# Kernel optimization log

Measured on AMD Instinct MI355X. Metric: run time of the kernel, lower is better.

## Reference

```python
import jax, jax.numpy as jnp
import numpy as np

B, T, U = 4, 256, 128
EH, PH, JH, V = 1024, 640, 640, 1024


def setup_inputs() -> dict:
    key = jax.random.key(0)
    ks = jax.random.split(key, 8)
    s_e = 1.0 / np.sqrt(EH)
    s_p = 1.0 / np.sqrt(PH)
    s_j = 1.0 / np.sqrt(JH)
    return {
        "enc": jax.random.normal(ks[0], (B, EH, T), jnp.float32),
        "dec": jax.random.normal(ks[1], (B, PH, U), jnp.float32),
        "W_enc": jax.random.uniform(ks[2], (JH, EH), jnp.float32, -s_e, s_e),
        "b_enc": jax.random.uniform(ks[3], (JH,), jnp.float32, -s_e, s_e),
        "W_pred": jax.random.uniform(ks[4], (JH, PH), jnp.float32, -s_p, s_p),
        "b_pred": jax.random.uniform(ks[5], (JH,), jnp.float32, -s_p, s_p),
        "W_out": jax.random.uniform(ks[6], (V, JH), jnp.float32, -s_j, s_j),
        "b_out": jax.random.uniform(ks[7], (V,), jnp.float32, -s_j, s_j),
    }


def reference(enc, dec, W_enc, b_enc, W_pred, b_pred, W_out, b_out):
    # enc: [B, EH, T], dec: [B, PH, U]  (channels-first, as in torch forward)
    # enc projection -> [B, T, JH] (transpose fused into einsum)
    e = jnp.einsum('bht,jh->btj', enc, W_enc) + b_enc
    # pred projection -> [B, U, JH]
    p = jnp.einsum('bhu,jh->buj', dec, W_pred) + b_pred
    # broadcast add -> [B, T, U, JH], ReLU, output projection -> [B, T, U, V]
    h = jax.nn.relu(e[:, :, None, :] + p[:, None, :, :])
    logits = jnp.einsum('btuj,vj->btuv', h, W_out) + b_out
    return jax.nn.log_softmax(logits, axis=-1)
```

## Files before the change

kernel.cpp:

```cpp
#include <hip/hip_runtime.h>
#include <hip/hip_bf16.h>
#include <stdint.h>

#define B_ 4
#define T_ 256
#define U_ 128
#define EH_ 1024
#define PH_ 640
#define JH_ 640
#define V_ 1024
#define KT_ 20

typedef short bf16x8 __attribute__((ext_vector_type(8)));
typedef float f32x4 __attribute__((ext_vector_type(4)));
typedef unsigned short u16;

typedef const __attribute__((address_space(1))) uint32_t cgu32_t;
typedef __attribute__((address_space(3))) uint32_t lu32_t;

__device__ __forceinline__ u16 f2bf(float f) {
  union { float f; uint32_t u; } v;
  v.f = f;
  uint32_t u = v.u;
  return (u16)((u + 0x7FFFu + ((u >> 16) & 1u)) >> 16);
}

__device__ __forceinline__ void gload16(const void* g, void* l) {
  __builtin_amdgcn_global_load_lds((cgu32_t*)g, (lu32_t*)l, 16, 0, 0);
}

#define VMW(n) asm volatile("s_waitcnt vmcnt(" #n ")" ::: "memory")
#define LGKM0  asm volatile("s_waitcnt lgkmcnt(0)" ::: "memory")
#define SCHEDB __builtin_amdgcn_sched_barrier(0)

__global__ void k_transpose_cvt(const float* __restrict__ in, u16* __restrict__ out,
                                int H, int W) {
  __shared__ float tile[32][33];
  int b = blockIdx.z;
  int h0 = blockIdx.y * 32, w0 = blockIdx.x * 32;
  const float* pin = in + (size_t)b * H * W;
  u16* pout = out + (size_t)b * H * W;
  int lw = threadIdx.x & 31, lh = threadIdx.x >> 5;
#pragma unroll
  for (int i = 0; i < 4; i++) {
    int h = lh + i * 8;
    tile[h][lw] = pin[(size_t)(h0 + h) * W + (w0 + lw)];
  }
  __syncthreads();
#pragma unroll
  for (int i = 0; i < 4; i++) {
    int w = lh + i * 8;
    pout[(size_t)(w0 + w) * H + (h0 + lw)] = f2bf(tile[lw][w]);
  }
}

__global__ void k_prep_w(const float* __restrict__ We, const float* __restrict__ Wp,
                         const float* __restrict__ Wo,
                         u16* __restrict__ WeB, u16* __restrict__ WpB,
                         u16* __restrict__ Wpk) {
  int s = blockIdx.x * 256 + threadIdx.x;
  if (s < 163840) {
    int idx = s * 4;
    float4 v = *(const float4*)(We + idx);
    ushort4 o;
    o.x = f2bf(v.x); o.y = f2bf(v.y); o.z = f2bf(v.z); o.w = f2bf(v.w);
    *(ushort4*)(WeB + idx) = o;
  } else if (s < 266240) {
    int idx = (s - 163840) * 4;
    float4 v = *(const float4*)(Wp + idx);
    ushort4 o;
    o.x = f2bf(v.x); o.y = f2bf(v.y); o.z = f2bf(v.z); o.w = f2bf(v.w);
    *(ushort4*)(WpB + idx) = o;
  } else {
    int q = s - 266240;
    int c = q & 1023;
    int g = (q >> 10) & 3;
    int t = q >> 12;
    const float* src = Wo + (size_t)c * JH_ + t * 32 + g * 8;
    float4 a = *(const float4*)src;
    float4 b2 = *(const float4*)(src + 4);
    ushort4 lo, hi;
    lo.x = f2bf(a.x);  lo.y = f2bf(a.y);  lo.z = f2bf(a.z);  lo.w = f2bf(a.w);
    hi.x = f2bf(b2.x); hi.y = f2bf(b2.y); hi.z = f2bf(b2.z); hi.w = f2bf(b2.w);
    u16* d = Wpk + (size_t)q * 8;
    *(ushort4*)d = lo;
    *(ushort4*)(d + 4) = hi;
  }
}

__global__ void k_proj_gemm(const u16* __restrict__ A, const u16* __restrict__ Bm,
                            const float* __restrict__ bias, float* __restrict__ C,
                            int K, int N, size_t strideA, size_t strideC) {
  __shared__ __align__(16) u16 sA[64 * 64];
  __shared__ __align__(16) u16 sB[64 * 64];
  int bb = blockIdx.z;
  const u16* Ab = A + (size_t)bb * strideA;
  float* Cb = C + (size_t)bb * strideC;
  int m0 = blockIdx.x * 64, n0 = blockIdx.y * 64;
  int tid = threadIdx.x;
  int lane = tid & 63, wid = tid >> 6;

  f32x4 acc[2][2] = {};
  for (int kk = 0; kk < K; kk += 64) {
#pragma unroll
    for (int i = 0; i < 2; i++) {
      int c = tid + i * 256;
      int r = c >> 3, kc = c & 7;
      int s = (r << 3) | (kc ^ (r & 7));
      *(bf16x8*)(sA + s * 8) = *(const bf16x8*)(Ab + (size_t)(m0 + r) * K + kk + kc * 8);
      *(bf16x8*)(sB + s * 8) = *(const bf16x8*)(Bm + (size_t)(n0 + r) * K + kk + kc * 8);
    }
    __syncthreads();
    int wr = (wid >> 1) * 32, wc = (wid & 1) * 32;
    int lr = lane & 15, lk = lane >> 4;
#pragma unroll
    for (int ki = 0; ki < 2; ki++) {
      bf16x8 af[2], bq[2];
#pragma unroll
      for (int mf = 0; mf < 2; mf++) {
        int r = wr + mf * 16 + lr;
        int kc = ki * 4 + lk;
        int s = (r << 3) | (kc ^ (r & 7));
        af[mf] = *(const bf16x8*)(sA + s * 8);
      }
#pragma unroll
      for (int nf = 0; nf < 2; nf++) {
        int r = wc + nf * 16 + lr;
        int kc = ki * 4 + lk;
        int s = (r << 3) | (kc ^ (r & 7));
        bq[nf] = *(const bf16x8*)(sB + s * 8);
      }
#pragma unroll
      for (int mf = 0; mf < 2; mf++)
#pragma unroll
        for (int nf = 0; nf < 2; nf++)
          acc[mf][nf] = __builtin_amdgcn_mfma_f32_16x16x32_bf16(af[mf], bq[nf], acc[mf][nf], 0, 0, 0);
    }
    __syncthreads();
  }
  int wr = (wid >> 1) * 32, wc = (wid & 1) * 32;
  int lr = lane & 15, lq = lane >> 4;
#pragma unroll
  for (int nf = 0; nf < 2; nf++) {
    int n = n0 + wc + nf * 16 + lr;
    float bv = bias[n];
#pragma unroll
    for (int mf = 0; mf < 2; mf++) {
#pragma unroll
      for (int r = 0; r < 4; r++) {
        int m = m0 + wr + mf * 16 + lq * 4 + r;
        Cb[(size_t)m * N + n] = acc[mf][nf][r] + bv;
      }
    }
  }
}

__global__ __launch_bounds__(512)
void k_fused(const float* __restrict__ e, const float* __restrict__ p,
             const u16* __restrict__ Wpk, const float* __restrict__ bout,
             float* __restrict__ out) {
  __shared__ __align__(16) u16 sB[2][32768];
  __shared__ __align__(16) u16 sA[4][2048];
  __shared__ __align__(16) float sE[JH_];
  __shared__ float redm[512];
  __shared__ float reds[512];

  int bid = blockIdx.x;
  int btile = bid >> 1, half = bid & 1, b = btile >> 8;
  int tid = threadIdx.x, lane = tid & 63, wn = tid >> 6;
  int lr = lane & 15, lk = lane >> 4;

  const float* eRow = e + (size_t)btile * JH_;
  const float* pRow = p + ((size_t)b * U_ + half * 64) * JH_;
  float* outB = out + ((size_t)btile * U_ + half * 64) * V_;

  int r_ = tid >> 3, kq_ = tid & 7;
  const float* pSrc = pRow + (size_t)r_ * JH_ + kq_ * 4;
  int aw = (kq_ >> 1) * 512 + r_ * 8 + (kq_ & 1) * 4;

  f32x4 acc[4][8] = {};

  auto stage = [&](int t, int c) {
    const u16* s0 = Wpk + (size_t)t * 32768 + (2 * wn) * 512 + lane * 8;
    u16* d0 = &sB[c][(2 * wn) * 512];
#pragma unroll
    for (int g = 0; g < 4; g++) {
      gload16(s0 + g * 8192, d0 + g * 8192);
      gload16(s0 + g * 8192 + 512, d0 + g * 8192 + 512);
    }
  };
  auto build = [&](int t, float4 pv) {
    float4 ev = *(const float4*)(&sE[t * 32 + kq_ * 4]);
    ushort4 hv;
    hv.x = f2bf(fmaxf(pv.x + ev.x, 0.f));
    hv.y = f2bf(fmaxf(pv.y + ev.y, 0.f));
    hv.z = f2bf(fmaxf(pv.z + ev.z, 0.f));
    hv.w = f2bf(fmaxf(pv.w + ev.w, 0.f));
    *(ushort4*)(&sA[t & 3][aw]) = hv;
  };

  for (int i = tid; i < JH_; i += 512) sE[i] = eRow[i];
  stage(0, 0);
  float4 pbuild = *(const float4*)(pSrc);
  float4 pnext  = *(const float4*)(pSrc + 32);
  LGKM0;
  __builtin_amdgcn_s_barrier();
  build(0, pbuild);
  pbuild = pnext;
  asm volatile("s_waitcnt vmcnt(0) lgkmcnt(0)" ::: "memory");
  __builtin_amdgcn_s_barrier();

  for (int t = 0; t < KT_; t++) {
    if (t + 1 < KT_) stage(t + 1, (t + 1) & 1);
    float4 pfut;
    if (t + 2 < KT_) pfut = *(const float4*)(pSrc + (t + 2) * 32);
    if (t + 1 < KT_) { build(t + 1, pbuild); pbuild = pfut; }
    SCHEDB;
    if (t < KT_ - 2) { VMW(9); } else if (t == KT_ - 2) { VMW(8); } else { VMW(0); }
    SCHEDB;
    __builtin_amdgcn_s_barrier();
    const u16* Ab = &sA[t & 3][lk * 512];
    const u16* Bb = &sB[t & 1][lk * 8192 + wn * 1024];
    bf16x8 af[4], bq[8];
#pragma unroll
    for (int mf = 0; mf < 4; mf++)
      af[mf] = *(const bf16x8*)(Ab + (mf * 16 + lr) * 8);
#pragma unroll
    for (int nf = 0; nf < 8; nf++)
      bq[nf] = *(const bf16x8*)(Bb + (nf * 16 + lr) * 8);
    LGKM0; SCHEDB;
    __builtin_amdgcn_s_setprio(1);
#pragma unroll
    for (int mf = 0; mf < 4; mf++)
#pragma unroll
      for (int nf = 0; nf < 8; nf++)
        acc[mf][nf] = __builtin_amdgcn_mfma_f32_16x16x32_bf16(af[mf], bq[nf], acc[mf][nf], 0, 0, 0);
    __builtin_amdgcn_s_setprio(0);
  }

  float bv[8];
#pragma unroll
  for (int nf = 0; nf < 8; nf++) bv[nf] = bout[wn * 128 + nf * 16 + lr];
#pragma unroll
  for (int mf = 0; mf < 4; mf++)
#pragma unroll
    for (int nf = 0; nf < 8; nf++)
#pragma unroll
      for (int r = 0; r < 4; r++)
        acc[mf][nf][r] += bv[nf];

  float gm[4][4];
#pragma unroll
  for (int mf = 0; mf < 4; mf++)
#pragma unroll
    for (int r = 0; r < 4; r++) {
      float m = acc[mf][0][r];
#pragma unroll
      for (int nf = 1; nf < 8; nf++) m = fmaxf(m, acc[mf][nf][r]);
#pragma unroll
      for (int o = 1; o < 16; o <<= 1) m = fmaxf(m, __shfl_xor(m, o, 64));
      gm[mf][r] = m;
    }
  if ((lane & 15) == 0) {
#pragma unroll
    for (int mf = 0; mf < 4; mf++)
#pragma unroll
      for (int r = 0; r < 4; r++)
        redm[(mf * 16 + lk * 4 + r) * 8 + wn] = gm[mf][r];
  }
  __syncthreads();
#pragma unroll
  for (int mf = 0; mf < 4; mf++)
#pragma unroll
    for (int r = 0; r < 4; r++) {
      int row = mf * 16 + lk * 4 + r;
      float m = redm[row * 8];
#pragma unroll
      for (int w = 1; w < 8; w++) m = fmaxf(m, redm[row * 8 + w]);
      gm[mf][r] = m;
    }
  float ls[4][4];
#pragma unroll
  for (int mf = 0; mf < 4; mf++)
#pragma unroll
    for (int r = 0; r < 4; r++) {
      float s = 0.f;
#pragma unroll
      for (int nf = 0; nf < 8; nf++) s += __expf(acc[mf][nf][r] - gm[mf][r]);
#pragma unroll
      for (int o = 1; o < 16; o <<= 1) s += __shfl_xor(s, o, 64);
      ls[mf][r] = s;
    }
  if ((lane & 15) == 0) {
#pragma unroll
    for (int mf = 0; mf < 4; mf++)
#pragma unroll
      for (int r = 0; r < 4; r++)
        reds[(mf * 16 + lk * 4 + r) * 8 + wn] = ls[mf][r];
  }
  __syncthreads();
#pragma unroll
  for (int mf = 0; mf < 4; mf++)
#pragma unroll
    for (int r = 0; r < 4; r++) {
      int row = mf * 16 + lk * 4 + r;
      float s = reds[row * 8];
#pragma unroll
      for (int w = 1; w < 8; w++) s += reds[row * 8 + w];
      ls[mf][r] = gm[mf][r] + __logf(s);
    }
#pragma unroll
  for (int mf = 0; mf < 4; mf++)
#pragma unroll
    for (int nf = 0; nf < 8; nf++)
#pragma unroll
      for (int r = 0; r < 4; r++)
        outB[(size_t)(mf * 16 + lk * 4 + r) * V_ + wn * 128 + nf * 16 + lr] =
            acc[mf][nf][r] - ls[mf][r];
}

extern "C" void kernel_launch(void* const* d_in, const int* in_sizes, int n_in,
                              void* d_out, int out_size, void* d_ws, size_t ws_size,
                              hipStream_t stream) {
  const float* enc    = (const float*)d_in[0];
  const float* dec    = (const float*)d_in[1];
  const float* W_enc  = (const float*)d_in[2];
  const float* b_enc  = (const float*)d_in[3];
  const float* W_pred = (const float*)d_in[4];
  const float* b_pred = (const float*)d_in[5];
  const float* W_out  = (const float*)d_in[6];
  const float* b_out  = (const float*)d_in[7];
  float* out = (float*)d_out;

  char* ws = (char*)d_ws;
  size_t off = 0;
  auto alloc = [&](size_t bytes) {
    void* pp = ws + off;
    off = (off + bytes + 255) & ~(size_t)255;
    return pp;
  };
  u16* encT   = (u16*)alloc((size_t)B_ * T_ * EH_ * 2);
  u16* decT   = (u16*)alloc((size_t)B_ * U_ * PH_ * 2);
  u16* WencB  = (u16*)alloc((size_t)JH_ * EH_ * 2);
  u16* WpredB = (u16*)alloc((size_t)JH_ * PH_ * 2);
  u16* Wpk    = (u16*)alloc((size_t)KT_ * 32768 * 2);
  float* eBuf = (float*)alloc((size_t)B_ * T_ * JH_ * 4);
  float* pBuf = (float*)alloc((size_t)B_ * U_ * JH_ * 4);

  k_transpose_cvt<<<dim3(T_ / 32, EH_ / 32, B_), 256, 0, stream>>>(enc, encT, EH_, T_);
  k_transpose_cvt<<<dim3(U_ / 32, PH_ / 32, B_), 256, 0, stream>>>(dec, decT, PH_, U_);
  k_prep_w<<<1360, 256, 0, stream>>>(W_enc, W_pred, W_out, WencB, WpredB, Wpk);
  k_proj_gemm<<<dim3(T_ / 64, JH_ / 64, B_), 256, 0, stream>>>(
      encT, WencB, b_enc, eBuf, EH_, JH_, (size_t)T_ * EH_, (size_t)T_ * JH_);
  k_proj_gemm<<<dim3(U_ / 64, JH_ / 64, B_), 256, 0, stream>>>(
      decT, WpredB, b_pred, pBuf, PH_, JH_, (size_t)U_ * PH_, (size_t)U_ * JH_);

  k_fused<<<B_ * T_ * 2, 512, 0, stream>>>(eBuf, pBuf, Wpk, b_out, out);
}
```

Before: 329.6 us.

## Load fused-kernel operands directly into registers, dropping LDS staging

The fused joint kernel no longer stages the W_out tiles and the ReLU activations through shared memory. Each wave now loads its W fragments and a repacked p tensor straight from global memory into registers, with double-buffered prefetch. A new pack kernel lays p out so the loads line up with the MFMA fragments, and the bf16 conversion now uses the packed v_cvt_pk_bf16_f32 instruction. This removes the LDS round trips and most barriers, but every wave fetches its own W data from global memory and cache, and register pressure goes up under launch_bounds(512,2).

```diff
diff --git a/kernel.cpp b/kernel.cpp
--- a/kernel.cpp
+++ b/kernel.cpp
@@ -15,9 +15,6 @@
 typedef float f32x4 __attribute__((ext_vector_type(4)));
 typedef unsigned short u16;
 
-typedef const __attribute__((address_space(1))) uint32_t cgu32_t;
-typedef __attribute__((address_space(3))) uint32_t lu32_t;
-
 __device__ __forceinline__ u16 f2bf(float f) {
   union { float f; uint32_t u; } v;
   v.f = f;
@@ -25,13 +22,11 @@
   return (u16)((u + 0x7FFFu + ((u >> 16) & 1u)) >> 16);
 }
 
-__device__ __forceinline__ void gload16(const void* g, void* l) {
-  __builtin_amdgcn_global_load_lds((cgu32_t*)g, (lu32_t*)l, 16, 0, 0);
-}
-
-#define VMW(n) asm volatile("s_waitcnt vmcnt(" #n ")" ::: "memory")
-#define LGKM0  asm volatile("s_waitcnt lgkmcnt(0)" ::: "memory")
-#define SCHEDB __builtin_amdgcn_sched_barrier(0)
+__device__ __forceinline__ uint32_t cvt2(float lo, float hi) {
+  uint32_t r;
+  asm("v_cvt_pk_bf16_f32 %0, %1, %2" : "=v"(r) : "v"(lo), "v"(hi));
+  return r;
+}
 
 __global__ void k_transpose_cvt(const float* __restrict__ in, u16* __restrict__ out,
                                 int H, int W) {
@@ -155,13 +150,23 @@
   }
 }
 
-__global__ __launch_bounds__(512)
-void k_fused(const float* __restrict__ e, const float* __restrict__ p,
-             const u16* __restrict__ Wpk, const float* __restrict__ bout,
-             float* __restrict__ out) {
-  __shared__ __align__(16) u16 sB[2][32768];
-  __shared__ __align__(16) u16 sA[4][2048];
-  __shared__ __align__(16) float sE[JH_];
+__global__ void k_pack_p(const float* __restrict__ pBuf, float* __restrict__ pPk) {
+  int s = blockIdx.x * 256 + threadIdx.x;
+  int m = s & 127;
+  int g = (s >> 7) % 80;
+  int b = (s >> 7) / 80;
+  const float* src = pBuf + ((size_t)b * 128 + m) * JH_ + g * 8;
+  float4 a = *(const float4*)src;
+  float4 c = *(const float4*)(src + 4);
+  float* d = pPk + (size_t)s * 8;
+  *(float4*)d = a;
+  *(float4*)(d + 4) = c;
+}
+
+__global__ __launch_bounds__(512, 2)
+void k_fused_reg(const float* __restrict__ e, const float* __restrict__ pPk,
+                 const u16* __restrict__ Wpk, const float* __restrict__ bout,
+                 float* __restrict__ out) {
   __shared__ float redm[512];
   __shared__ float reds[512];
 
@@ -171,71 +176,66 @@
   int lr = lane & 15, lk = lane >> 4;
 
   const float* eRow = e + (size_t)btile * JH_;
-  const float* pRow = p + ((size_t)b * U_ + half * 64) * JH_;
+  const float* pB0 = pPk + (((size_t)b * 80 * 128) + half * 64 + lr) * 8;
+  const u16* wB0 = Wpk + ((size_t)wn * 128 + lr) * 8;
   float* outB = out + ((size_t)btile * U_ + half * 64) * V_;
 
-  int r_ = tid >> 3, kq_ = tid & 7;
-  const float* pSrc = pRow + (size_t)r_ * JH_ + kq_ * 4;
-  int aw = (kq_ >> 1) * 512 + r_ * 8 + (kq_ & 1) * 4;
-
   f32x4 acc[4][8] = {};
-
-  auto stage = [&](int t, int c) {
-    const u16* s0 = Wpk + (size_t)t * 32768 + (2 * wn) * 512 + lane * 8;
-    u16* d0 = &sB[c][(2 * wn) * 512];
-#pragma unroll
-    for (int g = 0; g < 4; g++) {
-      gload16(s0 + g * 8192, d0 + g * 8192);
-      gload16(s0 + g * 8192 + 512, d0 + g * 8192 + 512);
-    }
-  };
-  auto build = [&](int t, float4 pv) {
-    float4 ev = *(const float4*)(&sE[t * 32 + kq_ * 4]);
-    ushort4 hv;
-    hv.x = f2bf(fmaxf(pv.x + ev.x, 0.f));
-    hv.y = f2bf(fmaxf(pv.y + ev.y, 0.f));
-    hv.z = f2bf(fmaxf(pv.z + ev.z, 0.f));
-    hv.w = f2bf(fmaxf(pv.w + ev.w, 0.f));
-    *(ushort4*)(&sA[t & 3][aw]) = hv;
-  };
-
-  for (int i = tid; i < JH_; i += 512) sE[i] = eRow[i];
-  stage(0, 0);
-  float4 pbuild = *(const float4*)(pSrc);
-  float4 pnext  = *(const float4*)(pSrc + 32);
-  LGKM0;
-  __builtin_amdgcn_s_barrier();
-  build(0, pbuild);
-  pbuild = pnext;
-  asm volatile("s_waitcnt vmcnt(0) lgkmcnt(0)" ::: "memory");
-  __builtin_amdgcn_s_barrier();
-
+  float4 pv[4][2];
+  float4 ev[2];
+  bf16x8 af[4];
+  bf16x8 bq[2][8];
+
+  auto loadE = [&](int t) {
+    const float* ep = eRow + t * 32 + lk * 8;
+    ev[0] = *(const float4*)ep;
+    ev[1] = *(const float4*)(ep + 4);
+  };
+  auto loadP = [&](int t) {
+#pragma unroll
+    for (int mf = 0; mf < 4; mf++) {
+      const float* pp = pB0 + ((size_t)(t * 4 + lk) * 128 + mf * 16) * 8;
+      pv[mf][0] = *(const float4*)pp;
+      pv[mf][1] = *(const float4*)(pp + 4);
+    }
+  };
+  auto loadB = [&](int t, bf16x8* d) {
+#pragma unroll
+    for (int nf = 0; nf < 8; nf++)
+      d[nf] = *(const bf16x8*)(wB0 + ((size_t)(t * 4 + lk) * 1024 + nf * 16) * 8);
+  };
+  auto buildA = [&]() {
+#pragma unroll
+    for (int mf = 0; mf < 4; mf++) {
+      union { uint32_t u[4]; bf16x8 v; } r;
+      r.u[0] = cvt2(fmaxf(pv[mf][0].x + ev[0].x, 0.f), fmaxf(pv[mf][0].y + ev[0].y, 0.f));
+      r.u[1] = cvt2(fmaxf(pv[mf][0].z + ev[0].z, 0.f), fmaxf(pv[mf][0].w + ev[0].w, 0.f));
+      r.u[2] = cvt2(fmaxf(pv[mf][1].x + ev[1].x, 0.f), fmaxf(pv[mf][1].y + ev[1].y, 0.f));
+      r.u[3] = cvt2(fmaxf(pv[mf][1].z + ev[1].z, 0.f), fmaxf(pv[mf][1].w + ev[1].w, 0.f));
+      af[mf] = r.v;
+    }
+  };
+
+  loadE(0);
+  loadP(0);
+  loadB(0, bq[0]);
+  buildA();
+
+#pragma unroll
   for (int t = 0; t < KT_; t++) {
-    if (t + 1 < KT_) stage(t + 1, (t + 1) & 1);
-    float4 pfut;
-    if (t + 2 < KT_) pfut = *(const float4*)(pSrc + (t + 2) * 32);
-    if (t + 1 < KT_) { build(t + 1, pbuild); pbuild = pfut; }
-    SCHEDB;
-    if (t < KT_ - 2) { VMW(9); } else if (t == KT_ - 2) { VMW(8); } else { VMW(0); }
-    SCHEDB;
-    __builtin_amdgcn_s_barrier();
-    const u16* Ab = &sA[t & 3][lk * 512];
-    const u16* Bb = &sB[t & 1][lk * 8192 + wn * 1024];
-    bf16x8 af[4], bq[8];
+    const int c = t & 1;
+    if (t + 1 < KT_) {
+      loadP(t + 1);
+      loadE(t + 1);
+      loadB(t + 1, bq[c ^ 1]);
+    }
 #pragma unroll
     for (int mf = 0; mf < 4; mf++)
-      af[mf] = *(const bf16x8*)(Ab + (mf * 16 + lr) * 8);
-#pragma unroll
-    for (int nf = 0; nf < 8; nf++)
-      bq[nf] = *(const bf16x8*)(Bb + (nf * 16 + lr) * 8);
-    LGKM0; SCHEDB;
-    __builtin_amdgcn_s_setprio(1);
-#pragma unroll
-    for (int mf = 0; mf < 4; mf++)
 #pragma unroll
       for (int nf = 0; nf < 8; nf++)
-        acc[mf][nf] = __builtin_amdgcn_mfma_f32_16x16x32_bf16(af[mf], bq[nf], acc[mf][nf], 0, 0, 0);
-    __builtin_amdgcn_s_setprio(0);
+        acc[mf][nf] = __builtin_amdgcn_mfma_f32_16x16x32_bf16(af[mf], bq[c][nf], acc[mf][nf], 0, 0, 0);
+    if (t + 1 < KT_) buildA();
+    if ((t & 1) == 1 && t + 1 < KT_) __builtin_amdgcn_s_barrier();
   }
 
   float bv[8];
@@ -346,6 +346,7 @@
   u16* Wpk    = (u16*)alloc((size_t)KT_ * 32768 * 2);
   float* eBuf = (float*)alloc((size_t)B_ * T_ * JH_ * 4);
   float* pBuf = (float*)alloc((size_t)B_ * U_ * JH_ * 4);
+  float* pPk  = (float*)alloc((size_t)B_ * 80 * 128 * 8 * 4);
 
   k_transpose_cvt<<<dim3(T_ / 32, EH_ / 32, B_), 256, 0, stream>>>(enc, encT, EH_, T_);
   k_transpose_cvt<<<dim3(U_ / 32, PH_ / 32, B_), 256, 0, stream>>>(dec, decT, PH_, U_);
@@ -354,6 +355,7 @@
       encT, WencB, b_enc, eBuf, EH_, JH_, (size_t)T_ * EH_, (size_t)T_ * JH_);
   k_proj_gemm<<<dim3(U_ / 64, JH_ / 64, B_), 256, 0, stream>>>(
       decT, WpredB, b_pred, pBuf, PH_, JH_, (size_t)U_ * PH_, (size_t)U_ * JH_);
-
-  k_fused<<<B_ * T_ * 2, 512, 0, stream>>>(eBuf, pBuf, Wpk, b_out, out);
-}
+  k_pack_p<<<160, 256, 0, stream>>>(pBuf, pPk);
+
+  k_fused_reg<<<B_ * T_ * 2, 512, 0, stream>>>(eBuf, pPk, Wpk, b_out, out);
+}
```

After: 437.1 us. 32.6% more time.

## Pack pred projection for coalesced loads, halve barriers, stagger K-tile start per block

Applied to the files above, without the earlier changes.

Adds a pack kernel that lays out the pred projection so each wave loads contiguous float4 chunks. The fused kernel now builds two K-tiles of the ReLU activation at once, so there is one barrier per two K-steps instead of one per step. Each block starts its K loop at a different phase to spread weight-tile reads across blocks. It also uses the packed bf16 convert instruction. In exchange it adds an extra kernel launch and a global buffer, and the wait counts are more complex and easier to get wrong.

```diff
diff --git a/kernel.cpp b/kernel.cpp
--- a/kernel.cpp
+++ b/kernel.cpp
@@ -23,6 +23,12 @@
   v.f = f;
   uint32_t u = v.u;
   return (u16)((u + 0x7FFFu + ((u >> 16) & 1u)) >> 16);
+}
+
+__device__ __forceinline__ uint32_t cvt2(float lo, float hi) {
+  uint32_t r;
+  asm("v_cvt_pk_bf16_f32 %0, %1, %2" : "=v"(r) : "v"(lo), "v"(hi));
+  return r;
 }
 
 __device__ __forceinline__ void gload16(const void* g, void* l) {
@@ -155,12 +161,24 @@
   }
 }
 
+__global__ void k_pack_p2(const float* __restrict__ pBuf, float* __restrict__ pPk) {
+  int s = blockIdx.x * 256 + threadIdx.x;
+  int bh = s / 10240;
+  int rem = s - bh * 10240;
+  int g4 = rem >> 6;
+  int r = rem & 63;
+  int b = bh >> 1, half = bh & 1;
+  const float* src = pBuf + ((size_t)(b * 128 + half * 64 + r)) * JH_ + g4 * 4;
+  float4 v = *(const float4*)src;
+  *(float4*)(pPk + (size_t)s * 4) = v;
+}
+
 __global__ __launch_bounds__(512)
-void k_fused(const float* __restrict__ e, const float* __restrict__ p,
-             const u16* __restrict__ Wpk, const float* __restrict__ bout,
-             float* __restrict__ out) {
+void k_fused3(const float* __restrict__ e, const float* __restrict__ pPk,
+              const u16* __restrict__ Wpk, const float* __restrict__ bout,
+              float* __restrict__ out) {
   __shared__ __align__(16) u16 sB[2][32768];
-  __shared__ __align__(16) u16 sA[4][2048];
+  __shared__ __align__(16) u16 sA[2][4096];
   __shared__ __align__(16) float sE[JH_];
   __shared__ float redm[512];
   __shared__ float reds[512];
@@ -169,19 +187,19 @@
   int btile = bid >> 1, half = bid & 1, b = btile >> 8;
   int tid = threadIdx.x, lane = tid & 63, wn = tid >> 6;
   int lr = lane & 15, lk = lane >> 4;
+  int ph = (bid % 10) * 2;
 
   const float* eRow = e + (size_t)btile * JH_;
-  const float* pRow = p + ((size_t)b * U_ + half * 64) * JH_;
+  const float* pPbase = pPk + ((size_t)(b * 2 + half) * 40960) + wn * 256 + lane * 4;
   float* outB = out + ((size_t)btile * U_ + half * 64) * V_;
 
-  int r_ = tid >> 3, kq_ = tid & 7;
-  const float* pSrc = pRow + (size_t)r_ * JH_ + kq_ * 4;
-  int aw = (kq_ >> 1) * 512 + r_ * 8 + (kq_ & 1) * 4;
+  int awr = (wn >> 1) * 512 + lane * 8 + (wn & 1) * 4;
 
   f32x4 acc[4][8] = {};
 
-  auto stage = [&](int t, int c) {
-    const u16* s0 = Wpk + (size_t)t * 32768 + (2 * wn) * 512 + lane * 8;
+  auto tp = [&](int t) { int x = t + ph; return x >= KT_ ? x - KT_ : x; };
+  auto stage = [&](int tph, int c) {
+    const u16* s0 = Wpk + (size_t)tph * 32768 + (2 * wn) * 512 + lane * 8;
     u16* d0 = &sB[c][(2 * wn) * 512];
 #pragma unroll
     for (int g = 0; g < 4; g++) {
@@ -189,37 +207,42 @@
       gload16(s0 + g * 8192 + 512, d0 + g * 8192 + 512);
     }
   };
-  auto build = [&](int t, float4 pv) {
-    float4 ev = *(const float4*)(&sE[t * 32 + kq_ * 4]);
-    ushort4 hv;
-    hv.x = f2bf(fmaxf(pv.x + ev.x, 0.f));
-    hv.y = f2bf(fmaxf(pv.y + ev.y, 0.f));
-    hv.z = f2bf(fmaxf(pv.z + ev.z, 0.f));
-    hv.w = f2bf(fmaxf(pv.w + ev.w, 0.f));
-    *(ushort4*)(&sA[t & 3][aw]) = hv;
+  auto loadp = [&](int tph) { return *(const float4*)(pPbase + tph * 2048); };
+  auto build = [&](int slot, int tin, int tph, float4 pv) {
+    float4 ev = *(const float4*)(&sE[tph * 32 + wn * 4]);
+    uint2 w;
+    w.x = cvt2(fmaxf(pv.x + ev.x, 0.f), fmaxf(pv.y + ev.y, 0.f));
+    w.y = cvt2(fmaxf(pv.z + ev.z, 0.f), fmaxf(pv.w + ev.w, 0.f));
+    *(uint2*)(&sA[slot][tin * 2048 + awr]) = w;
   };
 
   for (int i = tid; i < JH_; i += 512) sE[i] = eRow[i];
-  stage(0, 0);
-  float4 pbuild = *(const float4*)(pSrc);
-  float4 pnext  = *(const float4*)(pSrc + 32);
+  stage(tp(0), 0);
+  float4 p0  = loadp(tp(0));
+  float4 p1  = loadp(tp(1));
+  float4 pcA = loadp(tp(2));
+  float4 pcB = loadp(tp(3));
+  float4 pnA = p0, pnB = p0;
   LGKM0;
   __builtin_amdgcn_s_barrier();
-  build(0, pbuild);
-  pbuild = pnext;
+  build(0, 0, tp(0), p0);
+  build(0, 1, tp(1), p1);
   asm volatile("s_waitcnt vmcnt(0) lgkmcnt(0)" ::: "memory");
   __builtin_amdgcn_s_barrier();
 
+#pragma unroll
   for (int t = 0; t < KT_; t++) {
-    if (t + 1 < KT_) stage(t + 1, (t + 1) & 1);
-    float4 pfut;
-    if (t + 2 < KT_) pfut = *(const float4*)(pSrc + (t + 2) * 32);
-    if (t + 1 < KT_) { build(t + 1, pbuild); pbuild = pfut; }
+    if (t + 1 < KT_) stage(tp(t + 1), (t + 1) & 1);
+    if ((t & 1) == 0 && t + 4 < KT_) { pnA = loadp(tp(t + 4)); pnB = loadp(tp(t + 5)); }
+    if ((t & 1) == 0 && t + 2 < KT_) {
+      int q1 = ((t >> 1) + 1) & 1;
+      build(q1, 0, tp(t + 2), pcA);
+      build(q1, 1, tp(t + 3), pcB);
+    }
     SCHEDB;
-    if (t < KT_ - 2) { VMW(9); } else if (t == KT_ - 2) { VMW(8); } else { VMW(0); }
+    if (t <= 15) { VMW(10); } else if (t <= 18) { VMW(8); } else { VMW(0); }
     SCHEDB;
-    __builtin_amdgcn_s_barrier();
-    const u16* Ab = &sA[t & 3][lk * 512];
+    const u16* Ab = &sA[(t >> 1) & 1][(t & 1) * 2048 + lk * 512];
     const u16* Bb = &sB[t & 1][lk * 8192 + wn * 1024];
     bf16x8 af[4], bq[8];
 #pragma unroll
@@ -236,6 +259,11 @@
       for (int nf = 0; nf < 8; nf++)
         acc[mf][nf] = __builtin_amdgcn_mfma_f32_16x16x32_bf16(af[mf], bq[nf], acc[mf][nf], 0, 0, 0);
     __builtin_amdgcn_s_setprio(0);
+    if ((t & 1) && t + 1 < KT_) {
+      pcA = pnA; pcB = pnB;
+      LGKM0;
+      __builtin_amdgcn_s_barrier();
+    }
   }
 
   float bv[8];
@@ -346,6 +374,7 @@
   u16* Wpk    = (u16*)alloc((size_t)KT_ * 32768 * 2);
   float* eBuf = (float*)alloc((size_t)B_ * T_ * JH_ * 4);
   float* pBuf = (float*)alloc((size_t)B_ * U_ * JH_ * 4);
+  float* pPk  = (float*)alloc((size_t)81920 * 4 * 4);
 
   k_transpose_cvt<<<dim3(T_ / 32, EH_ / 32, B_), 256, 0, stream>>>(enc, encT, EH_, T_);
   k_transpose_cvt<<<dim3(U_ / 32, PH_ / 32, B_), 256, 0, stream>>>(dec, decT, PH_, U_);
@@ -354,6 +383,7 @@
       encT, WencB, b_enc, eBuf, EH_, JH_, (size_t)T_ * EH_, (size_t)T_ * JH_);
   k_proj_gemm<<<dim3(U_ / 64, JH_ / 64, B_), 256, 0, stream>>>(
       decT, WpredB, b_pred, pBuf, PH_, JH_, (size_t)U_ * PH_, (size_t)U_ * JH_);
-
-  k_fused<<<B_ * T_ * 2, 512, 0, stream>>>(eBuf, pBuf, Wpk, b_out, out);
-}
+  k_pack_p2<<<320, 256, 0, stream>>>(pBuf, pPk);
+
+  k_fused3<<<B_ * T_ * 2, 512, 0, stream>>>(eBuf, pPk, Wpk, b_out, out);
+}
```

After: 312.7 us. 1.05x faster.
